# Performance work log

Hardware: AMD Instinct MI355X
Metric: run time of the kernel (lower is better)

Reference implementation:

```python
import jax, jax.numpy as jnp
import numpy as np

DEPTH = 8
LEAVES = 2 ** DEPTH            # 256 leaf values
N_NODES = 2 ** DEPTH - 1       # 255 internal split nodes
TEMP = 1.0
EPS_P = 1e-5
EPS_V = 1e-10
EPS_MASK = 1e-12


def setup_inputs() -> dict:
    key = jax.random.key(0)
    k1, k2, k3 = jax.random.split(key, 3)
    B, D, O = 8192, 512, 64
    x = jax.random.normal(k1, (B, D), dtype=jnp.float32)
    # BaseSplitter assumed: single linear layer + temperature sigmoid
    Ws = jax.random.normal(k2, (D, N_NODES), dtype=jnp.float32) * (1.0 / np.sqrt(D))
    bs = jnp.zeros((N_NODES,), dtype=jnp.float32)
    # xavier_uniform_ init for leaf value table (LEAVES, O)
    limit = float(np.sqrt(6.0 / (LEAVES + O)))
    value = jax.random.uniform(k3, (LEAVES, O), dtype=jnp.float32, minval=-limit, maxval=limit)
    return {"x": x, "Ws": Ws, "bs": bs, "value": value}


def _sdt_forward(x, Ws, bs, value):
    B = x.shape[0]
    leaves = value.shape[0]
    # splitter: per-node routing probabilities, shape (B, 2^depth - 1)
    probs = jax.nn.sigmoid((x @ Ws + bs) / TEMP)

    accum = jnp.zeros((B, leaves), dtype=jnp.float32)
    reg = jnp.float32(0.0)
    for d in range(DEPTH):  # small fixed loop over tree depth
        s, e = 2 ** d - 1, 2 ** (d + 1) - 1
        p = probs[:, s:e]                     # (B, 2^d) nodes at depth d
        logp = jnp.log(jnp.clip(p, EPS_P))
        log1mp = jnp.log(jnp.clip(1.0 - p, EPS_P))
        # regularization: sum over nodes of mean over batch
        reg = reg + (-0.5) * (2.0 ** (-d)) * jnp.log(jnp.clip(p * (1.0 - p), EPS_P)).mean(axis=0).sum()
        # interleave [logp_i, log1mp_i] per node, then broadcast each entry
        # over its span of leaves/2^(d+1) leaf slots
        contrib = jnp.stack([logp, log1mp], axis=-1).reshape(B, 2 ** (d + 1))
        rep = leaves // (2 ** (d + 1))
        accum = accum + jnp.broadcast_to(contrib[:, :, None], (B, 2 ** (d + 1), rep)).reshape(B, leaves)

    sign = jnp.sign(value)                                    # (L, O)
    logval = jnp.log(jnp.clip(jnp.abs(value), EPS_V))          # (L, O)
    ret = logval[None, :, :] + accum[:, :, None]               # (B, L, O)
    log_pos = jax.nn.logsumexp(ret + jnp.log((sign > 0).astype(jnp.float32) + EPS_MASK), axis=1)
    log_neg = jax.nn.logsumexp(ret + jnp.log((sign < 0).astype(jnp.float32) + EPS_MASK), axis=1)
    out = jnp.exp(log_pos) - jnp.exp(log_neg)                  # (B, O)
    return out, reg


def reference(x, Ws, bs, value):
    return _sdt_forward(x, Ws, bs, value)
```

## Files before the change

### kernel.cpp

```cpp
#include <hip/hip_runtime.h>


typedef __attribute__((ext_vector_type(8))) _Float16 half8;
typedef __attribute__((ext_vector_type(4))) _Float16 half4;
typedef __attribute__((ext_vector_type(4))) float floatx4;

constexpr int O = 64;
constexpr int XSTR = 520;
constexpr int PSTR = 280;
constexpr int LSTR = 260;

__global__ __launch_bounds__(256) void sdt_pre(
    const float* __restrict__ Ws, const float* __restrict__ value,
    _Float16* __restrict__ wt, _Float16* __restrict__ vt,
    float* __restrict__ reg_slot)
{
  const int bid = blockIdx.x, t = threadIdx.x;
  if (bid < 64) {
    const int k0 = bid * 8;
    const int n = t;
    const int T = n >> 4, r = n & 15;
    const int c = k0 >> 5, q = (k0 >> 3) & 3;
    _Float16 v8[8];
#pragma unroll
    for (int kk = 0; kk < 8; ++kk) {
      float f = (n < 255) ? Ws[(size_t)(k0 + kk) * 255 + n] : 0.f;
      v8[kk] = (_Float16)f;
    }
    *(half8*)&wt[(size_t)(T * 16 + c) * 512 + (q * 16 + r) * 8] = *(half8*)v8;
  } else {
    const int k0 = (bid - 64) * 64;
#pragma unroll
    for (int j = 0; j < 16; ++j) {
      int e = t + j * 256;
      int k = k0 + (e >> 6), n = e & 63;
      float f = value[(size_t)k * O + n];
      int T = n >> 4, r = n & 15, kc = k >> 5, q = (k >> 3) & 3, jj = k & 7;
      vt[(size_t)(T * 8 + kc) * 512 + (q * 16 + r) * 8 + jj] = (_Float16)f;
    }
    if (bid == 64 && t == 0) *reg_slot = 0.f;
  }
}

__global__ __launch_bounds__(512, 1) void sdt_main(
    const float* __restrict__ x, const _Float16* __restrict__ wt,
    const _Float16* __restrict__ vt, const float* __restrict__ bs,
    float* __restrict__ out, float* __restrict__ reg_out)
{
  __shared__ __align__(16) char smem[33280 + 17920];
  _Float16* xh_s = (_Float16*)smem;
  float*    L_s  = (float*)smem;
  _Float16* P_h  = (_Float16*)(smem + 33280);
  __shared__ float red_s[8];

  const int t = threadIdx.x, lane = t & 63, w = t >> 6;
  const int q = lane >> 4, r16 = lane & 15;
  const int R0 = blockIdx.x * 32;

  const _Float16* pb0 = wt + (size_t)(2 * w) * 16 * 512 + lane * 8;
  const _Float16* pb1 = wt + (size_t)(2 * w + 1) * 16 * 512 + lane * 8;
  half8 Bs0[3][4], Bs1[3][4];
#pragma unroll
  for (int s = 0; s < 3; ++s)
#pragma unroll
    for (int j = 0; j < 4; ++j) {
      Bs0[s][j] = *(const half8*)(pb0 + (s * 4 + j) * 512);
      Bs1[s][j] = *(const half8*)(pb1 + (s * 4 + j) * 512);
    }

  {
    const int row = t >> 4, l4 = (t & 15) * 4;
    const float* xrow = x + (size_t)(R0 + row) * 512;
#pragma unroll
    for (int i = 0; i < 8; ++i) {
      const int k = l4 + i * 64;
      float4 v = *(const float4*)(xrow + k);
      half4 h = {(_Float16)v.x, (_Float16)v.y, (_Float16)v.z, (_Float16)v.w};
      *(half4*)&xh_s[row * XSTR + k] = h;
    }
  }
  __syncthreads();

  floatx4 acc00 = {0,0,0,0}, acc01 = {0,0,0,0}, acc10 = {0,0,0,0}, acc11 = {0,0,0,0};
  const int a0off = r16 * XSTR + q * 8, a1off = (16 + r16) * XSTR + q * 8;

#pragma unroll
  for (int g = 0; g < 4; ++g) {
    const int s = g % 3;
#pragma unroll
    for (int j = 0; j < 4; ++j) {
      const int c = g * 4 + j;
      half8 a0 = *(const half8*)&xh_s[a0off + c * 32];
      half8 a1 = *(const half8*)&xh_s[a1off + c * 32];
      half8 b0 = Bs0[s][j], b1 = Bs1[s][j];
      acc00 = __builtin_amdgcn_mfma_f32_16x16x32_f16(a0, b0, acc00, 0, 0, 0);
      acc01 = __builtin_amdgcn_mfma_f32_16x16x32_f16(a0, b1, acc01, 0, 0, 0);
      acc10 = __builtin_amdgcn_mfma_f32_16x16x32_f16(a1, b0, acc10, 0, 0, 0);
      acc11 = __builtin_amdgcn_mfma_f32_16x16x32_f16(a1, b1, acc11, 0, 0, 0);
    }
    if (g == 0) {
#pragma unroll
      for (int j = 0; j < 4; ++j) {
        Bs0[0][j] = *(const half8*)(pb0 + (12 + j) * 512);
        Bs1[0][j] = *(const half8*)(pb1 + (12 + j) * 512);
      }
    }
  }

  const int c0 = w * 32 + r16, c1 = c0 + 16;
  float pv00[4], pv01[4], pv10[4], pv11[4];
  float s0 = 0.f, s1 = 0.f;
  {
    const float b0 = bs[c0];
    const float b1 = (c1 < 255) ? bs[c1] : 0.f;
#pragma unroll
    for (int r = 0; r < 4; ++r) {
      float p;
      p = 1.f / (1.f + __expf(-(acc00[r] + b0))); pv00[r] = p;
      s0 += __logf(fmaxf(p * (1.f - p), 1e-5f));
      p = 1.f / (1.f + __expf(-(acc10[r] + b0))); pv10[r] = p;
      s0 += __logf(fmaxf(p * (1.f - p), 1e-5f));
      p = 1.f / (1.f + __expf(-(acc01[r] + b1))); pv01[r] = p;
      s1 += __logf(fmaxf(p * (1.f - p), 1e-5f));
      p = 1.f / (1.f + __expf(-(acc11[r] + b1))); pv11[r] = p;
      s1 += __logf(fmaxf(p * (1.f - p), 1e-5f));
    }
  }
  float rsum;
  {
    const int d0 = 31 - __clz(c0 + 1);
    rsum = s0 * (-0.5f / (8192.0f * (float)(1 << d0)));
    if (c1 < 255) {
      const int d1 = 31 - __clz(c1 + 1);
      rsum += s1 * (-0.5f / (8192.0f * (float)(1 << d1)));
    }
  }
#pragma unroll
  for (int off = 32; off; off >>= 1) rsum += __shfl_down(rsum, off, 64);

  __syncthreads();

  {
#pragma unroll
    for (int r = 0; r < 4; ++r) {
      const int row0 = q * 4 + r, row1 = row0 + 16;
      L_s[row0 * LSTR + c0] = pv00[r];
      L_s[row0 * LSTR + c1] = pv01[r];
      L_s[row1 * LSTR + c0] = pv10[r];
      L_s[row1 * LSTR + c1] = pv11[r];
    }
    if (lane == 0) red_s[w] = rsum;
  }
  __syncthreads();

  if (t == 0) {
    float s = 0.f;
#pragma unroll
    for (int i = 0; i < 8; ++i) s += red_s[i];
    atomicAdd(reg_out, s);
  }

  half8 VB[8];
  {
    const int tn = w >> 1;
    const _Float16* vb = vt + (size_t)(tn * 8) * 512 + lane * 8;
#pragma unroll
    for (int kc = 0; kc < 8; ++kc) VB[kc] = *(const half8*)(vb + kc * 512);
  }

  {
    const int g8 = t & 31, rp = t >> 5;
    const int Lb = g8 * 8;
#pragma unroll
    for (int rr = 0; rr < 2; ++rr) {
      const int row = rp * 2 + rr;
      const float* Lr = &L_s[row * LSTR];
      float pre = 1.f;
#pragma unroll
      for (int dd = 0; dd < 5; ++dd) {
        float p = Lr[(1 << dd) - 1 + (Lb >> (8 - dd))];
        float br = ((Lb >> (7 - dd)) & 1) ? (1.f - p) : p;
        pre *= fmaxf(br, 1e-5f);
      }
      float p5 = Lr[31 + g8];
      float s5a = fmaxf(p5, 1e-5f), s5b = fmaxf(1.f - p5, 1e-5f);
      float p6a = Lr[63 + 2 * g8], p6b = Lr[63 + 2 * g8 + 1];
      float p7v[4];
#pragma unroll
      for (int m = 0; m < 4; ++m) p7v[m] = Lr[127 + 4 * g8 + m];
      _Float16 ph[8];
#pragma unroll
      for (int j = 0; j < 8; ++j) {
        float s5 = (j & 4) ? s5b : s5a;
        float p6 = (j & 4) ? p6b : p6a;
        float s6 = fmaxf((j & 2) ? (1.f - p6) : p6, 1e-5f);
        float p7 = p7v[j >> 1];
        float s7 = fmaxf((j & 1) ? (1.f - p7) : p7, 1e-5f);
        ph[j] = (_Float16)(pre * s5 * s6 * s7);
      }
      *(half8*)&P_h[row * PSTR + Lb] = *(half8*)ph;
    }
  }
  __syncthreads();

  {
    const int tm = w & 1, tn = w >> 1;
    floatx4 C = {0, 0, 0, 0};
    const _Float16* pa = &P_h[(tm * 16 + r16) * PSTR + q * 8];
#pragma unroll
    for (int kc = 0; kc < 8; ++kc) {
      half8 A8 = *(const half8*)(pa + kc * 32);
      C = __builtin_amdgcn_mfma_f32_16x16x32_f16(A8, VB[kc], C, 0, 0, 0);
    }
    const int col = tn * 16 + r16;
#pragma unroll
    for (int r = 0; r < 4; ++r) {
      int row = tm * 16 + q * 4 + r;
      out[(size_t)(R0 + row) * O + col] = C[r];
    }
  }
}

extern "C" void kernel_launch(void* const* d_in, const int* in_sizes, int n_in,
                              void* d_out, int out_size, void* d_ws, size_t ws_size,
                              hipStream_t stream) {
  const float* x     = (const float*)d_in[0];
  const float* Ws    = (const float*)d_in[1];
  const float* bs    = (const float*)d_in[2];
  const float* value = (const float*)d_in[3];
  float* outp = (float*)d_out;
  float* reg_slot = outp + (size_t)8192 * O;
  _Float16* wt = (_Float16*)d_ws;
  _Float16* vt = wt + 256 * 512;

  sdt_pre<<<68, 256, 0, stream>>>(Ws, value, wt, vt, reg_slot);
  sdt_main<<<256, 512, 0, stream>>>(x, wt, vt, bs, outp, reg_slot);
}
```

Before: 82.48 us.

## Drop weight pre-pack kernel and load fp32 weights directly in main kernel

Removes the separate sdt_pre kernel that converted Ws and value to fp16 in an MFMA-friendly layout. The main kernel now gathers fp32 Ws and value with strided scalar loads, converts them to half in registers, and software-pipelines the Ws loads over a six-stage register ring. The reg slot is zeroed with hipMemsetAsync. This saves one kernel launch and a workspace round trip, but every block now issues many uncoalesced strided loads and holds many more registers.

Result: slower. 117.2 us (+42.1%).

```diff
diff --git a/kernel.cpp b/kernel.cpp
--- a/kernel.cpp
+++ b/kernel.cpp
@@ -10,41 +10,9 @@
 constexpr int PSTR = 280;
 constexpr int LSTR = 260;
 
-__global__ __launch_bounds__(256) void sdt_pre(
-    const float* __restrict__ Ws, const float* __restrict__ value,
-    _Float16* __restrict__ wt, _Float16* __restrict__ vt,
-    float* __restrict__ reg_slot)
-{
-  const int bid = blockIdx.x, t = threadIdx.x;
-  if (bid < 64) {
-    const int k0 = bid * 8;
-    const int n = t;
-    const int T = n >> 4, r = n & 15;
-    const int c = k0 >> 5, q = (k0 >> 3) & 3;
-    _Float16 v8[8];
-#pragma unroll
-    for (int kk = 0; kk < 8; ++kk) {
-      float f = (n < 255) ? Ws[(size_t)(k0 + kk) * 255 + n] : 0.f;
-      v8[kk] = (_Float16)f;
-    }
-    *(half8*)&wt[(size_t)(T * 16 + c) * 512 + (q * 16 + r) * 8] = *(half8*)v8;
-  } else {
-    const int k0 = (bid - 64) * 64;
-#pragma unroll
-    for (int j = 0; j < 16; ++j) {
-      int e = t + j * 256;
-      int k = k0 + (e >> 6), n = e & 63;
-      float f = value[(size_t)k * O + n];
-      int T = n >> 4, r = n & 15, kc = k >> 5, q = (k >> 3) & 3, jj = k & 7;
-      vt[(size_t)(T * 8 + kc) * 512 + (q * 16 + r) * 8 + jj] = (_Float16)f;
-    }
-    if (bid == 64 && t == 0) *reg_slot = 0.f;
-  }
-}
-
 __global__ __launch_bounds__(512, 1) void sdt_main(
-    const float* __restrict__ x, const _Float16* __restrict__ wt,
-    const _Float16* __restrict__ vt, const float* __restrict__ bs,
+    const float* __restrict__ x, const float* __restrict__ Ws,
+    const float* __restrict__ value, const float* __restrict__ bs,
     float* __restrict__ out, float* __restrict__ reg_out)
 {
   __shared__ __align__(16) char smem[33280 + 17920];
@@ -57,27 +25,34 @@
   const int q = lane >> 4, r16 = lane & 15;
   const int R0 = blockIdx.x * 32;
 
-  const _Float16* pb0 = wt + (size_t)(2 * w) * 16 * 512 + lane * 8;
-  const _Float16* pb1 = wt + (size_t)(2 * w + 1) * 16 * 512 + lane * 8;
-  half8 Bs0[3][4], Bs1[3][4];
-#pragma unroll
-  for (int s = 0; s < 3; ++s)
-#pragma unroll
-    for (int j = 0; j < 4; ++j) {
-      Bs0[s][j] = *(const half8*)(pb0 + (s * 4 + j) * 512);
-      Bs1[s][j] = *(const half8*)(pb1 + (s * 4 + j) * 512);
-    }
-
-  {
-    const int row = t >> 4, l4 = (t & 15) * 4;
-    const float* xrow = x + (size_t)(R0 + row) * 512;
-#pragma unroll
-    for (int i = 0; i < 8; ++i) {
-      const int k = l4 + i * 64;
-      float4 v = *(const float4*)(xrow + k);
-      half4 h = {(_Float16)v.x, (_Float16)v.y, (_Float16)v.z, (_Float16)v.w};
-      *(half4*)&xh_s[row * XSTR + k] = h;
-    }
+  const int col0 = w * 32 + r16, col1 = col0 + 16;
+  const bool v1 = (col1 < 255);
+  const float* pW0 = Ws + col0;
+  const float* pW1 = Ws + col1;
+
+  float raw[6][16];
+
+  const int xrowi = t >> 4, xl4 = (t & 15) * 4;
+  const float* xrow = x + (size_t)(R0 + xrowi) * 512;
+  float4 xv[8];
+#pragma unroll
+  for (int i = 0; i < 8; ++i) xv[i] = *(const float4*)(xrow + xl4 + i * 64);
+
+#pragma unroll
+  for (int s = 0; s < 6; ++s) {
+    const int kb = s * 32 + q * 8;
+#pragma unroll
+    for (int j = 0; j < 8; ++j) {
+      raw[s][j]     = pW0[(size_t)(kb + j) * 255];
+      raw[s][8 + j] = v1 ? pW1[(size_t)(kb + j) * 255] : 0.f;
+    }
+  }
+
+#pragma unroll
+  for (int i = 0; i < 8; ++i) {
+    half4 h = {(_Float16)xv[i].x, (_Float16)xv[i].y,
+               (_Float16)xv[i].z, (_Float16)xv[i].w};
+    *(half4*)&xh_s[xrowi * XSTR + xl4 + i * 64] = h;
   }
   __syncthreads();
 
@@ -85,34 +60,37 @@
   const int a0off = r16 * XSTR + q * 8, a1off = (16 + r16) * XSTR + q * 8;
 
 #pragma unroll
-  for (int g = 0; g < 4; ++g) {
-    const int s = g % 3;
-#pragma unroll
-    for (int j = 0; j < 4; ++j) {
-      const int c = g * 4 + j;
-      half8 a0 = *(const half8*)&xh_s[a0off + c * 32];
-      half8 a1 = *(const half8*)&xh_s[a1off + c * 32];
-      half8 b0 = Bs0[s][j], b1 = Bs1[s][j];
-      acc00 = __builtin_amdgcn_mfma_f32_16x16x32_f16(a0, b0, acc00, 0, 0, 0);
-      acc01 = __builtin_amdgcn_mfma_f32_16x16x32_f16(a0, b1, acc01, 0, 0, 0);
-      acc10 = __builtin_amdgcn_mfma_f32_16x16x32_f16(a1, b0, acc10, 0, 0, 0);
-      acc11 = __builtin_amdgcn_mfma_f32_16x16x32_f16(a1, b1, acc11, 0, 0, 0);
-    }
-    if (g == 0) {
-#pragma unroll
-      for (int j = 0; j < 4; ++j) {
-        Bs0[0][j] = *(const half8*)(pb0 + (12 + j) * 512);
-        Bs1[0][j] = *(const half8*)(pb1 + (12 + j) * 512);
+  for (int c = 0; c < 16; ++c) {
+    const int s = c % 6;
+    _Float16 b0e[8], b1e[8];
+#pragma unroll
+    for (int j = 0; j < 8; ++j) {
+      b0e[j] = (_Float16)raw[s][j];
+      b1e[j] = (_Float16)raw[s][8 + j];
+    }
+    half8 b0 = *(half8*)b0e, b1 = *(half8*)b1e;
+    if (c < 10) {
+      const int kb = (c + 6) * 32 + q * 8;
+#pragma unroll
+      for (int j = 0; j < 8; ++j) {
+        raw[s][j]     = pW0[(size_t)(kb + j) * 255];
+        raw[s][8 + j] = v1 ? pW1[(size_t)(kb + j) * 255] : 0.f;
       }
     }
-  }
-
-  const int c0 = w * 32 + r16, c1 = c0 + 16;
+    half8 a0 = *(const half8*)&xh_s[a0off + c * 32];
+    half8 a1 = *(const half8*)&xh_s[a1off + c * 32];
+    acc00 = __builtin_amdgcn_mfma_f32_16x16x32_f16(a0, b0, acc00, 0, 0, 0);
+    acc01 = __builtin_amdgcn_mfma_f32_16x16x32_f16(a0, b1, acc01, 0, 0, 0);
+    acc10 = __builtin_amdgcn_mfma_f32_16x16x32_f16(a1, b0, acc10, 0, 0, 0);
+    acc11 = __builtin_amdgcn_mfma_f32_16x16x32_f16(a1, b1, acc11, 0, 0, 0);
+  }
+
+  const int c0 = col0, c1 = col1;
   float pv00[4], pv01[4], pv10[4], pv11[4];
   float s0 = 0.f, s1 = 0.f;
   {
     const float b0 = bs[c0];
-    const float b1 = (c1 < 255) ? bs[c1] : 0.f;
+    const float b1 = v1 ? bs[c1] : 0.f;
 #pragma unroll
     for (int r = 0; r < 4; ++r) {
       float p;
@@ -130,7 +108,7 @@
   {
     const int d0 = 31 - __clz(c0 + 1);
     rsum = s0 * (-0.5f / (8192.0f * (float)(1 << d0)));
-    if (c1 < 255) {
+    if (v1) {
       const int d1 = 31 - __clz(c1 + 1);
       rsum += s1 * (-0.5f / (8192.0f * (float)(1 << d1)));
     }
@@ -160,12 +138,15 @@
     atomicAdd(reg_out, s);
   }
 
-  half8 VB[8];
-  {
-    const int tn = w >> 1;
-    const _Float16* vb = vt + (size_t)(tn * 8) * 512 + lane * 8;
-#pragma unroll
-    for (int kc = 0; kc < 8; ++kc) VB[kc] = *(const half8*)(vb + kc * 512);
+  const int tm = w & 1, tn = w >> 1;
+  float rawV[64];
+  {
+    const float* pV = value + tn * 16 + r16;
+#pragma unroll
+    for (int kc = 0; kc < 8; ++kc)
+#pragma unroll
+      for (int j = 0; j < 8; ++j)
+        rawV[kc * 8 + j] = pV[(size_t)(kc * 32 + q * 8 + j) * 64];
   }
 
   {
@@ -204,13 +185,16 @@
   __syncthreads();
 
   {
-    const int tm = w & 1, tn = w >> 1;
     floatx4 C = {0, 0, 0, 0};
     const _Float16* pa = &P_h[(tm * 16 + r16) * PSTR + q * 8];
 #pragma unroll
     for (int kc = 0; kc < 8; ++kc) {
+      _Float16 be[8];
+#pragma unroll
+      for (int j = 0; j < 8; ++j) be[j] = (_Float16)rawV[kc * 8 + j];
+      half8 B8 = *(half8*)be;
       half8 A8 = *(const half8*)(pa + kc * 32);
-      C = __builtin_amdgcn_mfma_f32_16x16x32_f16(A8, VB[kc], C, 0, 0, 0);
+      C = __builtin_amdgcn_mfma_f32_16x16x32_f16(A8, B8, C, 0, 0, 0);
     }
     const int col = tn * 16 + r16;
 #pragma unroll
@@ -230,9 +214,7 @@
   const float* value = (const float*)d_in[3];
   float* outp = (float*)d_out;
   float* reg_slot = outp + (size_t)8192 * O;
-  _Float16* wt = (_Float16*)d_ws;
-  _Float16* vt = wt + 256 * 512;
-
-  sdt_pre<<<68, 256, 0, stream>>>(Ws, value, wt, vt, reg_slot);
-  sdt_main<<<256, 512, 0, stream>>>(x, wt, vt, bs, outp, reg_slot);
+
+  hipMemsetAsync(reg_slot, 0, 4, stream);
+  sdt_main<<<256, 512, 0, stream>>>(x, Ws, value, bs, outp, reg_slot);
 }
```

## Double block size to 1024 threads and split GEMM rows across wave pairs

Applied to the files above, without the earlier changes.

The main kernel now launches 1024 threads per block (16 waves) instead of 512. Each wave computes a 16-row by 32-column tile of the splitter GEMM instead of 32x32, with a rolling prefetch of the weight fragments. Each thread also builds one leaf-probability row instead of two. Only half the waves take part in the final value GEMM. The aim is more latency hiding per CU, at the cost of loading each B fragment twice per block and leaving half the waves idle in the last stage.

Measured after the change: 83.57 us. No clear change (+1.3%).

```diff
diff --git a/kernel.cpp b/kernel.cpp
--- a/kernel.cpp
+++ b/kernel.cpp
@@ -42,7 +42,7 @@
   }
 }
 
-__global__ __launch_bounds__(512, 1) void sdt_main(
+__global__ __launch_bounds__(1024, 1) void sdt_main(
     const float* __restrict__ x, const _Float16* __restrict__ wt,
     const _Float16* __restrict__ vt, const float* __restrict__ bs,
     float* __restrict__ out, float* __restrict__ reg_out)
@@ -51,78 +51,65 @@
   _Float16* xh_s = (_Float16*)smem;
   float*    L_s  = (float*)smem;
   _Float16* P_h  = (_Float16*)(smem + 33280);
-  __shared__ float red_s[8];
+  __shared__ float red_s[16];
 
   const int t = threadIdx.x, lane = t & 63, w = t >> 6;
   const int q = lane >> 4, r16 = lane & 15;
   const int R0 = blockIdx.x * 32;
-
-  const _Float16* pb0 = wt + (size_t)(2 * w) * 16 * 512 + lane * 8;
-  const _Float16* pb1 = wt + (size_t)(2 * w + 1) * 16 * 512 + lane * 8;
-  half8 Bs0[3][4], Bs1[3][4];
-#pragma unroll
-  for (int s = 0; s < 3; ++s)
-#pragma unroll
-    for (int j = 0; j < 4; ++j) {
-      Bs0[s][j] = *(const half8*)(pb0 + (s * 4 + j) * 512);
-      Bs1[s][j] = *(const half8*)(pb1 + (s * 4 + j) * 512);
-    }
-
-  {
-    const int row = t >> 4, l4 = (t & 15) * 4;
-    const float* xrow = x + (size_t)(R0 + row) * 512;
-#pragma unroll
-    for (int i = 0; i < 8; ++i) {
-      const int k = l4 + i * 64;
-      float4 v = *(const float4*)(xrow + k);
-      half4 h = {(_Float16)v.x, (_Float16)v.y, (_Float16)v.z, (_Float16)v.w};
-      *(half4*)&xh_s[row * XSTR + k] = h;
-    }
-  }
-  __syncthreads();
-
-  floatx4 acc00 = {0,0,0,0}, acc01 = {0,0,0,0}, acc10 = {0,0,0,0}, acc11 = {0,0,0,0};
-  const int a0off = r16 * XSTR + q * 8, a1off = (16 + r16) * XSTR + q * 8;
-
-#pragma unroll
-  for (int g = 0; g < 4; ++g) {
-    const int s = g % 3;
-#pragma unroll
-    for (int j = 0; j < 4; ++j) {
-      const int c = g * 4 + j;
-      half8 a0 = *(const half8*)&xh_s[a0off + c * 32];
-      half8 a1 = *(const half8*)&xh_s[a1off + c * 32];
-      half8 b0 = Bs0[s][j], b1 = Bs1[s][j];
-      acc00 = __builtin_amdgcn_mfma_f32_16x16x32_f16(a0, b0, acc00, 0, 0, 0);
-      acc01 = __builtin_amdgcn_mfma_f32_16x16x32_f16(a0, b1, acc01, 0, 0, 0);
-      acc10 = __builtin_amdgcn_mfma_f32_16x16x32_f16(a1, b0, acc10, 0, 0, 0);
-      acc11 = __builtin_amdgcn_mfma_f32_16x16x32_f16(a1, b1, acc11, 0, 0, 0);
-    }
-    if (g == 0) {
-#pragma unroll
-      for (int j = 0; j < 4; ++j) {
-        Bs0[0][j] = *(const half8*)(pb0 + (12 + j) * 512);
-        Bs1[0][j] = *(const half8*)(pb1 + (12 + j) * 512);
-      }
-    }
-  }
-
-  const int c0 = w * 32 + r16, c1 = c0 + 16;
-  float pv00[4], pv01[4], pv10[4], pv11[4];
+  const int w_m = w >> 3, w_n = w & 7;
+
+  const int xrow_i = t >> 5, xcid = t & 31;
+  const float* xrow = x + (size_t)(R0 + xrow_i) * 512;
+  float4 xv[4];
+#pragma unroll
+  for (int i = 0; i < 4; ++i)
+    xv[i] = *(const float4*)(xrow + xcid * 4 + i * 128);
+
+  const _Float16* pb0 = wt + (size_t)(2 * w_n) * 16 * 512 + lane * 8;
+  const _Float16* pb1 = wt + (size_t)(2 * w_n + 1) * 16 * 512 + lane * 8;
+  half8 Bv0[8], Bv1[8];
+#pragma unroll
+  for (int c = 0; c < 8; ++c) {
+    Bv0[c] = *(const half8*)(pb0 + c * 512);
+    Bv1[c] = *(const half8*)(pb1 + c * 512);
+  }
+
+#pragma unroll
+  for (int i = 0; i < 4; ++i) {
+    half4 h = {(_Float16)xv[i].x, (_Float16)xv[i].y,
+               (_Float16)xv[i].z, (_Float16)xv[i].w};
+    *(half4*)&xh_s[xrow_i * XSTR + xcid * 4 + i * 128] = h;
+  }
+  __syncthreads();
+
+  floatx4 acc0 = {0,0,0,0}, acc1 = {0,0,0,0};
+  const int aoff = (w_m * 16 + r16) * XSTR + q * 8;
+
+#pragma unroll
+  for (int c = 0; c < 16; ++c) {
+    half8 b0 = Bv0[c & 7], b1 = Bv1[c & 7];
+    if (c < 8) {
+      Bv0[c & 7] = *(const half8*)(pb0 + (c + 8) * 512);
+      Bv1[c & 7] = *(const half8*)(pb1 + (c + 8) * 512);
+    }
+    half8 a = *(const half8*)&xh_s[aoff + c * 32];
+    acc0 = __builtin_amdgcn_mfma_f32_16x16x32_f16(a, b0, acc0, 0, 0, 0);
+    acc1 = __builtin_amdgcn_mfma_f32_16x16x32_f16(a, b1, acc1, 0, 0, 0);
+  }
+
+  const int c0 = w_n * 32 + r16, c1 = c0 + 16;
+  const bool v1ok = (c1 < 255);
+  float pv0[4], pv1[4];
   float s0 = 0.f, s1 = 0.f;
   {
     const float b0 = bs[c0];
-    const float b1 = (c1 < 255) ? bs[c1] : 0.f;
+    const float b1 = v1ok ? bs[c1] : 0.f;
 #pragma unroll
     for (int r = 0; r < 4; ++r) {
       float p;
-      p = 1.f / (1.f + __expf(-(acc00[r] + b0))); pv00[r] = p;
+      p = 1.f / (1.f + __expf(-(acc0[r] + b0))); pv0[r] = p;
       s0 += __logf(fmaxf(p * (1.f - p), 1e-5f));
-      p = 1.f / (1.f + __expf(-(acc10[r] + b0))); pv10[r] = p;
-      s0 += __logf(fmaxf(p * (1.f - p), 1e-5f));
-      p = 1.f / (1.f + __expf(-(acc01[r] + b1))); pv01[r] = p;
-      s1 += __logf(fmaxf(p * (1.f - p), 1e-5f));
-      p = 1.f / (1.f + __expf(-(acc11[r] + b1))); pv11[r] = p;
+      p = 1.f / (1.f + __expf(-(acc1[r] + b1))); pv1[r] = p;
       s1 += __logf(fmaxf(p * (1.f - p), 1e-5f));
     }
   }
@@ -130,7 +117,7 @@
   {
     const int d0 = 31 - __clz(c0 + 1);
     rsum = s0 * (-0.5f / (8192.0f * (float)(1 << d0)));
-    if (c1 < 255) {
+    if (v1ok) {
       const int d1 = 31 - __clz(c1 + 1);
       rsum += s1 * (-0.5f / (8192.0f * (float)(1 << d1)));
     }
@@ -143,11 +130,9 @@
   {
 #pragma unroll
     for (int r = 0; r < 4; ++r) {
-      const int row0 = q * 4 + r, row1 = row0 + 16;
-      L_s[row0 * LSTR + c0] = pv00[r];
-      L_s[row0 * LSTR + c1] = pv01[r];
-      L_s[row1 * LSTR + c0] = pv10[r];
-      L_s[row1 * LSTR + c1] = pv11[r];
+      const int row = w_m * 16 + q * 4 + r;
+      L_s[row * LSTR + c0] = pv0[r];
+      L_s[row * LSTR + c1] = pv1[r];
     }
     if (lane == 0) red_s[w] = rsum;
   }
@@ -156,12 +141,12 @@
   if (t == 0) {
     float s = 0.f;
 #pragma unroll
-    for (int i = 0; i < 8; ++i) s += red_s[i];
+    for (int i = 0; i < 16; ++i) s += red_s[i];
     atomicAdd(reg_out, s);
   }
 
   half8 VB[8];
-  {
+  if (w < 8) {
     const int tn = w >> 1;
     const _Float16* vb = vt + (size_t)(tn * 8) * 512 + lane * 8;
 #pragma unroll
@@ -169,41 +154,37 @@
   }
 
   {
-    const int g8 = t & 31, rp = t >> 5;
+    const int g8 = t & 31, row = t >> 5;
     const int Lb = g8 * 8;
-#pragma unroll
-    for (int rr = 0; rr < 2; ++rr) {
-      const int row = rp * 2 + rr;
-      const float* Lr = &L_s[row * LSTR];
-      float pre = 1.f;
-#pragma unroll
-      for (int dd = 0; dd < 5; ++dd) {
-        float p = Lr[(1 << dd) - 1 + (Lb >> (8 - dd))];
-        float br = ((Lb >> (7 - dd)) & 1) ? (1.f - p) : p;
-        pre *= fmaxf(br, 1e-5f);
-      }
-      float p5 = Lr[31 + g8];
-      float s5a = fmaxf(p5, 1e-5f), s5b = fmaxf(1.f - p5, 1e-5f);
-      float p6a = Lr[63 + 2 * g8], p6b = Lr[63 + 2 * g8 + 1];
-      float p7v[4];
-#pragma unroll
-      for (int m = 0; m < 4; ++m) p7v[m] = Lr[127 + 4 * g8 + m];
-      _Float16 ph[8];
-#pragma unroll
-      for (int j = 0; j < 8; ++j) {
-        float s5 = (j & 4) ? s5b : s5a;
-        float p6 = (j & 4) ? p6b : p6a;
-        float s6 = fmaxf((j & 2) ? (1.f - p6) : p6, 1e-5f);
-        float p7 = p7v[j >> 1];
-        float s7 = fmaxf((j & 1) ? (1.f - p7) : p7, 1e-5f);
-        ph[j] = (_Float16)(pre * s5 * s6 * s7);
-      }
-      *(half8*)&P_h[row * PSTR + Lb] = *(half8*)ph;
-    }
-  }
-  __syncthreads();
-
-  {
+    const float* Lr = &L_s[row * LSTR];
+    float pre = 1.f;
+#pragma unroll
+    for (int dd = 0; dd < 5; ++dd) {
+      float p = Lr[(1 << dd) - 1 + (Lb >> (8 - dd))];
+      float br = ((Lb >> (7 - dd)) & 1) ? (1.f - p) : p;
+      pre *= fmaxf(br, 1e-5f);
+    }
+    float p5 = Lr[31 + g8];
+    float s5a = fmaxf(p5, 1e-5f), s5b = fmaxf(1.f - p5, 1e-5f);
+    float p6a = Lr[63 + 2 * g8], p6b = Lr[63 + 2 * g8 + 1];
+    float p7v[4];
+#pragma unroll
+    for (int m = 0; m < 4; ++m) p7v[m] = Lr[127 + 4 * g8 + m];
+    _Float16 ph[8];
+#pragma unroll
+    for (int j = 0; j < 8; ++j) {
+      float s5 = (j & 4) ? s5b : s5a;
+      float p6 = (j & 4) ? p6b : p6a;
+      float s6 = fmaxf((j & 2) ? (1.f - p6) : p6, 1e-5f);
+      float p7 = p7v[j >> 1];
+      float s7 = fmaxf((j & 1) ? (1.f - p7) : p7, 1e-5f);
+      ph[j] = (_Float16)(pre * s5 * s6 * s7);
+    }
+    *(half8*)&P_h[row * PSTR + Lb] = *(half8*)ph;
+  }
+  __syncthreads();
+
+  if (w < 8) {
     const int tm = w & 1, tn = w >> 1;
     floatx4 C = {0, 0, 0, 0};
     const _Float16* pa = &P_h[(tm * 16 + r16) * PSTR + q * 8];
@@ -234,5 +215,5 @@
   _Float16* vt = wt + 256 * 512;
 
   sdt_pre<<<68, 256, 0, stream>>>(Ws, value, wt, vt, reg_slot);
-  sdt_main<<<256, 512, 0, stream>>>(x, wt, vt, bs, outp, reg_slot);
+  sdt_main<<<256, 1024, 0, stream>>>(x, wt, vt, bs, outp, reg_slot);
 }
```

## Issue x loads before weight loads, hold all B fragments, give L_s its own buffer

Applied to the files above, without the earlier changes.

The main kernel now issues its global loads of the x tile into registers before loading the weight fragments, then converts x to fp16 in shared memory afterwards. It keeps all 16 B fragments per wave resident in registers instead of a 3-stage rotating buffer, so the GEMM loop runs without mid-loop refills. L_s gets its own shared-memory region so the barrier between the GEMM and the probability stores can be dropped. The prep kernel moves to 512 threads per block with half the work per thread. The tradeoffs are higher register pressure from 32 half8 B fragments plus 8 float4 x values, and more LDS per block (about 84 KB).

Measured after the change: 81.91 us. About the same (-0.7%).

```diff
diff --git a/kernel.cpp b/kernel.cpp
--- a/kernel.cpp
+++ b/kernel.cpp
@@ -10,7 +10,7 @@
 constexpr int PSTR = 280;
 constexpr int LSTR = 260;
 
-__global__ __launch_bounds__(256) void sdt_pre(
+__global__ __launch_bounds__(512) void sdt_pre(
     const float* __restrict__ Ws, const float* __restrict__ value,
     _Float16* __restrict__ wt, _Float16* __restrict__ vt,
     float* __restrict__ reg_slot)
@@ -18,21 +18,23 @@
   const int bid = blockIdx.x, t = threadIdx.x;
   if (bid < 64) {
     const int k0 = bid * 8;
-    const int n = t;
+    const int n = t & 255, hf = t >> 8;
     const int T = n >> 4, r = n & 15;
     const int c = k0 >> 5, q = (k0 >> 3) & 3;
-    _Float16 v8[8];
-#pragma unroll
-    for (int kk = 0; kk < 8; ++kk) {
+    _Float16 v4h[4];
+#pragma unroll
+    for (int i = 0; i < 4; ++i) {
+      const int kk = hf * 4 + i;
       float f = (n < 255) ? Ws[(size_t)(k0 + kk) * 255 + n] : 0.f;
-      v8[kk] = (_Float16)f;
-    }
-    *(half8*)&wt[(size_t)(T * 16 + c) * 512 + (q * 16 + r) * 8] = *(half8*)v8;
+      v4h[i] = (_Float16)f;
+    }
+    *(half4*)&wt[(size_t)(T * 16 + c) * 512 + (q * 16 + r) * 8 + hf * 4] =
+        *(half4*)v4h;
   } else {
     const int k0 = (bid - 64) * 64;
 #pragma unroll
-    for (int j = 0; j < 16; ++j) {
-      int e = t + j * 256;
+    for (int j = 0; j < 8; ++j) {
+      int e = t + j * 512;
       int k = k0 + (e >> 6), n = e & 63;
       float f = value[(size_t)k * O + n];
       int T = n >> 4, r = n & 15, kc = k >> 5, q = (k >> 3) & 3, jj = k & 7;
@@ -47,37 +49,36 @@
     const _Float16* __restrict__ vt, const float* __restrict__ bs,
     float* __restrict__ out, float* __restrict__ reg_out)
 {
-  __shared__ __align__(16) char smem[33280 + 17920];
+  __shared__ __align__(16) char smem[33280 + 33280 + 17920];
   _Float16* xh_s = (_Float16*)smem;
-  float*    L_s  = (float*)smem;
-  _Float16* P_h  = (_Float16*)(smem + 33280);
+  float*    L_s  = (float*)(smem + 33280);
+  _Float16* P_h  = (_Float16*)(smem + 66560);
   __shared__ float red_s[8];
 
   const int t = threadIdx.x, lane = t & 63, w = t >> 6;
   const int q = lane >> 4, r16 = lane & 15;
   const int R0 = blockIdx.x * 32;
 
+  const int xrowi = t >> 4, xl4 = (t & 15) * 4;
+  const float* xrow = x + (size_t)(R0 + xrowi) * 512;
+  float4 xv[8];
+#pragma unroll
+  for (int i = 0; i < 8; ++i) xv[i] = *(const float4*)(xrow + xl4 + i * 64);
+
   const _Float16* pb0 = wt + (size_t)(2 * w) * 16 * 512 + lane * 8;
   const _Float16* pb1 = wt + (size_t)(2 * w + 1) * 16 * 512 + lane * 8;
-  half8 Bs0[3][4], Bs1[3][4];
-#pragma unroll
-  for (int s = 0; s < 3; ++s)
-#pragma unroll
-    for (int j = 0; j < 4; ++j) {
-      Bs0[s][j] = *(const half8*)(pb0 + (s * 4 + j) * 512);
-      Bs1[s][j] = *(const half8*)(pb1 + (s * 4 + j) * 512);
-    }
-
-  {
-    const int row = t >> 4, l4 = (t & 15) * 4;
-    const float* xrow = x + (size_t)(R0 + row) * 512;
-#pragma unroll
-    for (int i = 0; i < 8; ++i) {
-      const int k = l4 + i * 64;
-      float4 v = *(const float4*)(xrow + k);
-      half4 h = {(_Float16)v.x, (_Float16)v.y, (_Float16)v.z, (_Float16)v.w};
-      *(half4*)&xh_s[row * XSTR + k] = h;
-    }
+  half8 B0[16], B1[16];
+#pragma unroll
+  for (int c = 0; c < 16; ++c) {
+    B0[c] = *(const half8*)(pb0 + c * 512);
+    B1[c] = *(const half8*)(pb1 + c * 512);
+  }
+
+#pragma unroll
+  for (int i = 0; i < 8; ++i) {
+    half4 h = {(_Float16)xv[i].x, (_Float16)xv[i].y,
+               (_Float16)xv[i].z, (_Float16)xv[i].w};
+    *(half4*)&xh_s[xrowi * XSTR + xl4 + i * 64] = h;
   }
   __syncthreads();
 
@@ -85,34 +86,22 @@
   const int a0off = r16 * XSTR + q * 8, a1off = (16 + r16) * XSTR + q * 8;
 
 #pragma unroll
-  for (int g = 0; g < 4; ++g) {
-    const int s = g % 3;
-#pragma unroll
-    for (int j = 0; j < 4; ++j) {
-      const int c = g * 4 + j;
-      half8 a0 = *(const half8*)&xh_s[a0off + c * 32];
-      half8 a1 = *(const half8*)&xh_s[a1off + c * 32];
-      half8 b0 = Bs0[s][j], b1 = Bs1[s][j];
-      acc00 = __builtin_amdgcn_mfma_f32_16x16x32_f16(a0, b0, acc00, 0, 0, 0);
-      acc01 = __builtin_amdgcn_mfma_f32_16x16x32_f16(a0, b1, acc01, 0, 0, 0);
-      acc10 = __builtin_amdgcn_mfma_f32_16x16x32_f16(a1, b0, acc10, 0, 0, 0);
-      acc11 = __builtin_amdgcn_mfma_f32_16x16x32_f16(a1, b1, acc11, 0, 0, 0);
-    }
-    if (g == 0) {
-#pragma unroll
-      for (int j = 0; j < 4; ++j) {
-        Bs0[0][j] = *(const half8*)(pb0 + (12 + j) * 512);
-        Bs1[0][j] = *(const half8*)(pb1 + (12 + j) * 512);
-      }
-    }
+  for (int c = 0; c < 16; ++c) {
+    half8 a0 = *(const half8*)&xh_s[a0off + c * 32];
+    half8 a1 = *(const half8*)&xh_s[a1off + c * 32];
+    acc00 = __builtin_amdgcn_mfma_f32_16x16x32_f16(a0, B0[c], acc00, 0, 0, 0);
+    acc01 = __builtin_amdgcn_mfma_f32_16x16x32_f16(a0, B1[c], acc01, 0, 0, 0);
+    acc10 = __builtin_amdgcn_mfma_f32_16x16x32_f16(a1, B0[c], acc10, 0, 0, 0);
+    acc11 = __builtin_amdgcn_mfma_f32_16x16x32_f16(a1, B1[c], acc11, 0, 0, 0);
   }
 
   const int c0 = w * 32 + r16, c1 = c0 + 16;
+  const bool v1ok = (c1 < 255);
   float pv00[4], pv01[4], pv10[4], pv11[4];
   float s0 = 0.f, s1 = 0.f;
   {
     const float b0 = bs[c0];
-    const float b1 = (c1 < 255) ? bs[c1] : 0.f;
+    const float b1 = v1ok ? bs[c1] : 0.f;
 #pragma unroll
     for (int r = 0; r < 4; ++r) {
       float p;
@@ -130,15 +119,13 @@
   {
     const int d0 = 31 - __clz(c0 + 1);
     rsum = s0 * (-0.5f / (8192.0f * (float)(1 << d0)));
-    if (c1 < 255) {
+    if (v1ok) {
       const int d1 = 31 - __clz(c1 + 1);
       rsum += s1 * (-0.5f / (8192.0f * (float)(1 << d1)));
     }
   }
 #pragma unroll
   for (int off = 32; off; off >>= 1) rsum += __shfl_down(rsum, off, 64);
-
-  __syncthreads();
 
   {
 #pragma unroll
@@ -233,6 +220,6 @@
   _Float16* wt = (_Float16*)d_ws;
   _Float16* vt = wt + 256 * 512;
 
-  sdt_pre<<<68, 256, 0, stream>>>(Ws, value, wt, vt, reg_slot);
+  sdt_pre<<<68, 512, 0, stream>>>(Ws, value, wt, vt, reg_slot);
   sdt_main<<<256, 512, 0, stream>>>(x, wt, vt, bs, outp, reg_slot);
 }
```
